# Kernel tuning notes

Hardware: AMD Instinct MI355X
Metric: run time of the kernel (lower is better)

The kernel has to match this reference:

```python
import jax, jax.numpy as jnp
import numpy as np

# Module constants (from init_kwargs / source constants)
BEV_H, BEV_W = 188, 126
IMG_H, IMG_W = 384, 768
X_MIN, X_MAX = 0.0, 75.2
Y_MIN, Y_MAX = -25.2, 25.2


def _bev_points():
    """Homogeneous car-frame BEV cell centers, [P,4] with P = BEV_H*BEV_W, Z=0."""
    dx = (X_MAX - X_MIN) / BEV_H
    dy = (Y_MAX - Y_MIN) / BEV_W
    xc = jnp.linspace(X_MIN + dx / 2.0, X_MAX - dx / 2.0, BEV_H)
    yc = jnp.linspace(Y_MIN + dy / 2.0, Y_MAX - dy / 2.0, BEV_W)
    X, Y = jnp.meshgrid(xc, yc, indexing='ij')
    P = BEV_H * BEV_W
    return jnp.stack([X.ravel(), Y.ravel(), jnp.zeros(P), jnp.ones(P)], axis=-1)


def setup_inputs() -> dict:
    key = jax.random.key(0)
    k1, k2, k3 = jax.random.split(key, 3)
    B, N, C, Hf, Wf = 2, 6, 256, 48, 96
    feats = jax.random.normal(k1, (B, N, C, Hf, Wf), dtype=jnp.float32)
    # Realistic intrinsics: fx=fy=500, principal point at image center, + small noise
    K_base = jnp.array([[500.0, 0.0, IMG_W / 2.0],
                        [0.0, 500.0, IMG_H / 2.0],
                        [0.0, 0.0, 1.0]], dtype=jnp.float32)
    intrinsics = K_base[None, None] + 5.0 * jax.random.normal(k2, (B, N, 3, 3), dtype=jnp.float32)
    intrinsics = intrinsics.at[..., 2, :].set(jnp.array([0.0, 0.0, 1.0]))
    # Extrinsics: car x (forward) -> cam z, car y -> -cam x, car z (up) -> -cam y,
    # camera 1.5m above ground; small per-camera perturbation so cams differ.
    M_base = jnp.array([[0.0, -1.0, 0.0, 0.0],
                        [0.0, 0.0, -1.0, 1.5],
                        [1.0, 0.0, 0.0, 0.0],
                        [0.0, 0.0, 0.0, 1.0]], dtype=jnp.float32)
    car_to_cam = M_base[None, None] + 0.01 * jax.random.normal(k3, (B, N, 4, 4), dtype=jnp.float32)
    car_to_cam = car_to_cam.at[..., 3, :].set(jnp.array([0.0, 0.0, 0.0, 1.0]))
    return {"feats": feats, "intrinsics": intrinsics, "car_to_cam": car_to_cam}


def _forward(feats, intrinsics, car_to_cam):
    B, N, C, Hf, Wf = feats.shape
    P_car = _bev_points().astype(feats.dtype)  # [P,4]
    # Per-camera projection of BEV points into camera frame: P_cam = P_car @ M^T
    P_cam = jnp.einsum('pk,bnjk->bnpj', P_car, car_to_cam)  # [B,N,P,4]
    Zc = P_cam[..., 2]
    valid = Zc > 0.1
    # Pinhole projection: p_img = K @ P_cam3
    p_img = jnp.einsum('bnij,bnpj->bnpi', intrinsics, P_cam[..., :3])  # [B,N,P,3]
    z = jnp.maximum(p_img[..., 2], 1e-4)
    u_feat = (p_img[..., 0] / z) / (IMG_W / float(Wf))
    v_feat = (p_img[..., 1] / z) / (IMG_H / float(Hf))
    valid = valid & (u_feat >= 0.0) & (u_feat <= Wf - 1.0) & (v_feat >= 0.0) & (v_feat <= Hf - 1.0)
    u_norm = jnp.where(valid, u_feat / (Wf - 1) * 2.0 - 1.0, 2.0)
    v_norm = jnp.where(valid, v_feat / (Hf - 1) * 2.0 - 1.0, 2.0)
    # grid_sample, bilinear, padding_mode='zeros', align_corners=True
    ix = (u_norm + 1.0) * 0.5 * (Wf - 1)  # [B,N,P]
    iy = (v_norm + 1.0) * 0.5 * (Hf - 1)
    x0 = jnp.floor(ix)
    y0 = jnp.floor(iy)
    wx1 = ix - x0
    wx0 = 1.0 - wx1
    wy1 = iy - y0
    wy0 = 1.0 - wy1
    feats_flat = feats.reshape(B, N, C, Hf * Wf)

    def gather(xf, yf):
        inb = (xf >= 0) & (xf <= Wf - 1) & (yf >= 0) & (yf <= Hf - 1)
        xi = jnp.clip(xf, 0, Wf - 1).astype(jnp.int32)
        yi = jnp.clip(yf, 0, Hf - 1).astype(jnp.int32)
        lin = yi * Wf + xi  # [B,N,P]
        val = jnp.take_along_axis(feats_flat, lin[:, :, None, :], axis=3)  # [B,N,C,P]
        return val * inb[:, :, None, :].astype(val.dtype)

    out = (gather(x0, y0) * (wx0 * wy0)[:, :, None, :]
           + gather(x0 + 1.0, y0) * (wx1 * wy0)[:, :, None, :]
           + gather(x0, y0 + 1.0) * (wx0 * wy1)[:, :, None, :]
           + gather(x0 + 1.0, y0 + 1.0) * (wx1 * wy1)[:, :, None, :])  # [B,N,C,P]
    bev = out.mean(axis=1).reshape(B, C, BEV_H, BEV_W)
    return bev


def reference(feats, intrinsics, car_to_cam):
    return _forward(feats, intrinsics, car_to_cam)
```

## Files before the change

### kernel.cpp

```cpp
#include <hip/hip_runtime.h>

namespace {

constexpr int kBevH = 188, kBevW = 126, kP = kBevH * kBevW;
constexpr int kB = 2, kN = 6, kC = 256, kHf = 48, kWf = 96;
constexpr int kHW = kHf * kWf;
constexpr int kPixBytes = kC * 2;
constexpr int kPTile = 32;
constexpr int kNTiles = (kP + kPTile - 1) / kPTile;
constexpr size_t kImgBytes  = (size_t)kB * kN * kHW * kC * 2;
constexpr size_t kRecCount  = (size_t)kB * kP * (size_t)kN;
constexpr size_t kOffsBytes = kRecCount * 8;
constexpr size_t kWtsBytes  = kRecCount * 16;
constexpr size_t kWsNeeded  = kImgBytes + kOffsBytes + kWtsBytes;

__device__ __forceinline__ unsigned short f2bf(float f) {
  union { float f; unsigned u; } a; a.f = f;
  unsigned r = a.u + 0x7fffu + ((a.u >> 16) & 1u);
  return (unsigned short)(r >> 16);
}
__device__ __forceinline__ float bfl(unsigned u) {
  union { unsigned u; float f; } a; a.u = u << 16; return a.f;
}
__device__ __forceinline__ float bfh(unsigned u) {
  union { unsigned u; float f; } a; a.u = u & 0xffff0000u; return a.f;
}

__global__ __launch_bounds__(256) void taps_kernel(
    const float* __restrict__ intr, const float* __restrict__ c2c,
    int2* __restrict__ offs, float4* __restrict__ wts) {
  const int gid = blockIdx.x * 256 + threadIdx.x;
  if (gid >= kB * kP) return;
  const int b = gid / kP, p = gid - b * kP;
  const int pi = p / kBevW, pj = p - pi * kBevW;
  const float dx = 75.2f / 188.0f, dy = 50.4f / 126.0f;
  const float xcar = 0.5f * dx + (float)pi * dx;
  const float ycar = -25.2f + 0.5f * dy + (float)pj * dy;
  const float* Kb = intr + (size_t)b * kN * 9;
  const float* Mb = c2c + (size_t)b * kN * 16;
#pragma unroll
  for (int n = 0; n < kN; ++n) {
    const float* M = Mb + n * 16;
    const float* K = Kb + n * 9;
    float Xc = M[0] * xcar + M[1] * ycar + M[3];
    float Yc = M[4] * xcar + M[5] * ycar + M[7];
    float Zc = M[8] * xcar + M[9] * ycar + M[11];
    float u = K[0] * Xc + K[1] * Yc + K[2] * Zc;
    float v = K[3] * Xc + K[4] * Yc + K[5] * Zc;
    float w = K[6] * Xc + K[7] * Yc + K[8] * Zc;
    float z = fmaxf(w, 1e-4f);
    float uf = (u / z) * 0.125f;
    float vf = (v / z) * 0.125f;
    bool valid = (Zc > 0.1f) && (uf >= 0.0f) && (uf <= 95.0f) &&
                 (vf >= 0.0f) && (vf <= 47.0f);
    int2 ov = make_int2(0, 0);
    float4 wv = make_float4(0.f, 0.f, 0.f, 0.f);
    if (valid) {
      float un = (uf / 95.0f) * 2.0f - 1.0f;
      float vn = (vf / 47.0f) * 2.0f - 1.0f;
      float ix = (un + 1.0f) * 0.5f * 95.0f;
      float iy = (vn + 1.0f) * 0.5f * 47.0f;
      float x0f = floorf(ix), y0f = floorf(iy);
      float wx1 = ix - x0f, wx0 = 1.0f - wx1;
      float wy1 = iy - y0f, wy0 = 1.0f - wy1;
      int x0i = (int)x0f;
      int y0i = (int)y0f;
      int xb = min(x0i, 94);
      float h0 = (x0i <= 94) ? wx0 : 0.0f;
      float h1 = (x0i <= 94) ? wx1 : wx0;
      int y1i = min(y0i + 1, 47);
      const int pix = (b * kN + n) * kHW;
      ov.x = (pix + y0i * kWf + xb) * kPixBytes;
      ov.y = (pix + y1i * kWf + xb) * kPixBytes;
      wv = make_float4(h0 * wy0, h1 * wy0, h0 * wy1, h1 * wy1);
    }
    offs[(size_t)gid * kN + n] = ov;
    wts[(size_t)gid * kN + n] = wv;
  }
}

__global__ __launch_bounds__(256) void transpose_cvt_kernel(
    const float* __restrict__ src, unsigned short* __restrict__ dst) {
  __shared__ float tile[64][33];
  const int m = blockIdx.z;
  const int hw0 = blockIdx.x * 32;
  const int c0 = blockIdx.y * 64;
  const float* s = src + (size_t)m * kC * kHW;
  unsigned short* d = dst + (size_t)m * kHW * kC;
  const int hw = threadIdx.x & 31, cl = threadIdx.x >> 5;
#pragma unroll
  for (int k = 0; k < 8; ++k)
    tile[cl + 8 * k][hw] = s[(size_t)(c0 + cl + 8 * k) * kHW + hw0 + hw];
  __syncthreads();
  const int cp = threadIdx.x & 31, hwl = threadIdx.x >> 5;
#pragma unroll
  for (int k = 0; k < 4; ++k) {
    const int h = hwl + 8 * k;
    ushort2 uv;
    uv.x = f2bf(tile[2 * cp][h]);
    uv.y = f2bf(tile[2 * cp + 1][h]);
    *(ushort2*)(d + (size_t)(hw0 + h) * kC + c0 + 2 * cp) = uv;
  }
}

__global__ __launch_bounds__(512) void gather_kernel(
    const unsigned char* __restrict__ tf, const int2* __restrict__ offs,
    const float4* __restrict__ wts, float* __restrict__ out) {
  __shared__ float sm[kPTile][261];
  const int b = blockIdx.y;
  const int orig = blockIdx.x;
  constexpr int q = kNTiles / 8, r = kNTiles % 8;
  const int xcd = orig & 7, idx = orig >> 3;
  const int tile = (xcd < r ? xcd * (q + 1) : r * (q + 1) + (xcd - r) * q) + idx;
  const int p0 = tile * kPTile;
  const int tid = threadIdx.x;
  const int w = tid >> 6, l = tid & 63;
  const int half = l >> 5;
  const int l16 = l << 4;
  const float inv_n = 1.0f / 6.0f;

#pragma unroll 2
  for (int j = 0; j < 4; ++j) {
    const int pl = w * 4 + j;
    const int p = min(p0 + pl, kP - 1);
    int rec = (b * kP + p) * kN;
    rec = __builtin_amdgcn_readfirstlane(rec);

    const int2 o0 = offs[rec + 0], o1 = offs[rec + 1], o2 = offs[rec + 2],
               o3 = offs[rec + 3], o4 = offs[rec + 4], o5 = offs[rec + 5];
    const float4 w0 = wts[rec + 0], w1 = wts[rec + 1], w2 = wts[rec + 2],
                 w3 = wts[rec + 3], w4 = wts[rec + 4], w5 = wts[rec + 5];

#define LD(nm, o) \
    const uint4 nm##a = *(const uint4*)(tf + (size_t)o.x + l16); \
    const uint4 nm##b = *(const uint4*)(tf + (size_t)o.y + l16);
    LD(d0, o0) LD(d1, o1) LD(d2, o2) LD(d3, o3) LD(d4, o4) LD(d5, o5)
#undef LD

    float a0 = 0.f, a1 = 0.f, a2 = 0.f, a3 = 0.f,
          a4 = 0.f, a5 = 0.f, a6 = 0.f, a7 = 0.f;
#define CAM(nm, wv) { \
    const float wA = half ? wv.y : wv.x; \
    const float wB = half ? wv.w : wv.z; \
    a0 += wA * bfl(nm##a.x) + wB * bfl(nm##b.x); \
    a1 += wA * bfh(nm##a.x) + wB * bfh(nm##b.x); \
    a2 += wA * bfl(nm##a.y) + wB * bfl(nm##b.y); \
    a3 += wA * bfh(nm##a.y) + wB * bfh(nm##b.y); \
    a4 += wA * bfl(nm##a.z) + wB * bfl(nm##b.z); \
    a5 += wA * bfh(nm##a.z) + wB * bfh(nm##b.z); \
    a6 += wA * bfl(nm##a.w) + wB * bfl(nm##b.w); \
    a7 += wA * bfh(nm##a.w) + wB * bfh(nm##b.w); }
    CAM(d0, w0) CAM(d1, w1) CAM(d2, w2) CAM(d3, w3) CAM(d4, w4) CAM(d5, w5)
#undef CAM

    a0 += __shfl_xor(a0, 32); a1 += __shfl_xor(a1, 32);
    a2 += __shfl_xor(a2, 32); a3 += __shfl_xor(a3, 32);
    a4 += __shfl_xor(a4, 32); a5 += __shfl_xor(a5, 32);
    a6 += __shfl_xor(a6, 32); a7 += __shfl_xor(a7, 32);

    const int cbase = ((l & 31) << 3) + (half << 2);
    float4 vs = half ? make_float4(a4, a5, a6, a7)
                     : make_float4(a0, a1, a2, a3);
    vs.x *= inv_n; vs.y *= inv_n; vs.z *= inv_n; vs.w *= inv_n;
    *(float4*)&sm[pl][cbase] = vs;
  }
  __syncthreads();

#pragma unroll
  for (int rd = 0; rd < 4; ++rd) {
    const int cr = rd * 64 + (tid >> 3);
    const int p4 = (tid & 7) * 4;
    const int pg = p0 + p4;
    if (pg < kP) {
      float4 v = make_float4(sm[p4][cr], sm[p4 + 1][cr], sm[p4 + 2][cr],
                             sm[p4 + 3][cr]);
      *(float4*)(out + ((size_t)(b * kC + cr)) * kP + pg) = v;
    }
  }
}

constexpr int kCChunk = 32;
__global__ __launch_bounds__(256) void ipm_project_kernel(
    const float* __restrict__ feats, const float* __restrict__ intr,
    const float* __restrict__ c2c, float* __restrict__ out) {
  const int p = blockIdx.x * 256 + threadIdx.x;
  const int b = blockIdx.y;
  const int c0 = blockIdx.z * kCChunk;
  const bool inrange = p < kP;
  const int pi = p / kBevW;
  const int pj = p - pi * kBevW;
  const float dx = 75.2f / 188.0f;
  const float dy = 50.4f / 126.0f;
  const float xcar = 0.5f * dx + (float)pi * dx;
  const float ycar = -25.2f + 0.5f * dy + (float)pj * dy;
  int tap[kN][4];
  float tw[kN][4];
  int vmask = 0;
  const float* Kb = intr + (size_t)b * kN * 9;
  const float* Mb = c2c + (size_t)b * kN * 16;
#pragma unroll
  for (int n = 0; n < kN; ++n) {
    const float* M = Mb + n * 16;
    const float* K = Kb + n * 9;
    float Xc = M[0] * xcar + M[1] * ycar + M[3];
    float Yc = M[4] * xcar + M[5] * ycar + M[7];
    float Zc = M[8] * xcar + M[9] * ycar + M[11];
    float u = K[0] * Xc + K[1] * Yc + K[2] * Zc;
    float v = K[3] * Xc + K[4] * Yc + K[5] * Zc;
    float w = K[6] * Xc + K[7] * Yc + K[8] * Zc;
    float z = fmaxf(w, 1e-4f);
    float uf = (u / z) * 0.125f;
    float vf = (v / z) * 0.125f;
    bool valid = inrange && (Zc > 0.1f) && (uf >= 0.0f) && (uf <= 95.0f) &&
                 (vf >= 0.0f) && (vf <= 47.0f);
    if (valid) {
      float un = (uf / 95.0f) * 2.0f - 1.0f;
      float vn = (vf / 47.0f) * 2.0f - 1.0f;
      float ix = (un + 1.0f) * 0.5f * 95.0f;
      float iy = (vn + 1.0f) * 0.5f * 47.0f;
      float x0f = floorf(ix), y0f = floorf(iy);
      float wx1 = ix - x0f, wx0 = 1.0f - wx1;
      float wy1 = iy - y0f, wy0 = 1.0f - wy1;
#pragma unroll
      for (int t = 0; t < 4; ++t) {
        float xf = x0f + (float)(t & 1);
        float yf = y0f + (float)(t >> 1);
        bool inb =
            (xf >= 0.0f) && (xf <= 95.0f) && (yf >= 0.0f) && (yf <= 47.0f);
        int xi = (int)fminf(fmaxf(xf, 0.0f), 95.0f);
        int yi = (int)fminf(fmaxf(yf, 0.0f), 47.0f);
        float wgt = ((t & 1) ? wx1 : wx0) * ((t >> 1) ? wy1 : wy0);
        tap[n][t] = yi * kWf + xi;
        tw[n][t] = inb ? wgt : 0.0f;
      }
      vmask |= (1 << n);
    }
  }
  const float inv_n = 1.0f / 6.0f;
#pragma unroll 4
  for (int k = 0; k < kCChunk; ++k) {
    const int c = c0 + k;
    float acc = 0.0f;
#pragma unroll
    for (int n = 0; n < kN; ++n) {
      if (vmask & (1 << n)) {
        const float* f = feats + ((size_t)(b * kN + n) * kC + c) * kHW;
        acc += f[tap[n][0]] * tw[n][0] + f[tap[n][1]] * tw[n][1] +
               f[tap[n][2]] * tw[n][2] + f[tap[n][3]] * tw[n][3];
      }
    }
    if (inrange) out[((size_t)b * kC + c) * kP + p] = acc * inv_n;
  }
}

}

extern "C" void kernel_launch(void* const* d_in, const int* in_sizes, int n_in,
                              void* d_out, int out_size, void* d_ws,
                              size_t ws_size, hipStream_t stream) {
  const float* feats = (const float*)d_in[0];
  const float* intr = (const float*)d_in[1];
  const float* c2c = (const float*)d_in[2];
  float* out = (float*)d_out;

  if (ws_size >= kWsNeeded && d_ws != nullptr) {
    unsigned char* wsb = (unsigned char*)d_ws;
    unsigned short* tf = (unsigned short*)wsb;
    int2* offs = (int2*)(wsb + kImgBytes);
    float4* wtsp = (float4*)(wsb + kImgBytes + kOffsBytes);

    taps_kernel<<<(kB * kP + 255) / 256, 256, 0, stream>>>(intr, c2c, offs,
                                                           wtsp);
    transpose_cvt_kernel<<<dim3(kHW / 32, kC / 64, kB * kN), 256, 0, stream>>>(
        feats, tf);
    gather_kernel<<<dim3(kNTiles, kB), 512, 0, stream>>>(
        (const unsigned char*)tf, offs, wtsp, out);
  } else {
    dim3 grid((kP + 255) / 256, kB, kC / kCChunk);
    ipm_project_kernel<<<grid, dim3(256), 0, stream>>>(feats, intr, c2c, out);
  }
}
```

Measured before the change: 54.29 us.

## Fuse tap computation into gather kernel via shared memory, drop taps pass

Removes the separate taps kernel and computes per-point, per-camera offsets and bilinear weights inside the gather kernel. The first 192 threads of each block fill shared-memory arrays, and the rest of the block reads them after a barrier. This drops one kernel launch and the global write and read of the offset and weight records. It also fully unrolls the point loop and switches the output writes to nontemporal stores. The cost is a serial projection phase plus a barrier at the start of every gather block, and higher register pressure from the full unroll.

```diff
diff --git a/kernel.cpp b/kernel.cpp
--- a/kernel.cpp
+++ b/kernel.cpp
@@ -8,11 +8,10 @@
 constexpr int kPixBytes = kC * 2;
 constexpr int kPTile = 32;
 constexpr int kNTiles = (kP + kPTile - 1) / kPTile;
-constexpr size_t kImgBytes  = (size_t)kB * kN * kHW * kC * 2;
-constexpr size_t kRecCount  = (size_t)kB * kP * (size_t)kN;
-constexpr size_t kOffsBytes = kRecCount * 8;
-constexpr size_t kWtsBytes  = kRecCount * 16;
-constexpr size_t kWsNeeded  = kImgBytes + kOffsBytes + kWtsBytes;
+constexpr size_t kImgBytes = (size_t)kB * kN * kHW * kC * 2;
+constexpr size_t kWsNeeded = kImgBytes;
+
+typedef float vfloat4 __attribute__((ext_vector_type(4)));
 
 __device__ __forceinline__ unsigned short f2bf(float f) {
   union { float f; unsigned u; } a; a.f = f;
@@ -26,22 +25,54 @@
   union { unsigned u; float f; } a; a.u = u & 0xffff0000u; return a.f;
 }
 
-__global__ __launch_bounds__(256) void taps_kernel(
-    const float* __restrict__ intr, const float* __restrict__ c2c,
-    int2* __restrict__ offs, float4* __restrict__ wts) {
-  const int gid = blockIdx.x * 256 + threadIdx.x;
-  if (gid >= kB * kP) return;
-  const int b = gid / kP, p = gid - b * kP;
-  const int pi = p / kBevW, pj = p - pi * kBevW;
-  const float dx = 75.2f / 188.0f, dy = 50.4f / 126.0f;
-  const float xcar = 0.5f * dx + (float)pi * dx;
-  const float ycar = -25.2f + 0.5f * dy + (float)pj * dy;
-  const float* Kb = intr + (size_t)b * kN * 9;
-  const float* Mb = c2c + (size_t)b * kN * 16;
-#pragma unroll
-  for (int n = 0; n < kN; ++n) {
-    const float* M = Mb + n * 16;
-    const float* K = Kb + n * 9;
+__global__ __launch_bounds__(256) void transpose_cvt_kernel(
+    const float* __restrict__ src, unsigned short* __restrict__ dst) {
+  __shared__ float tile[64][33];
+  const int m = blockIdx.z;
+  const int hw0 = blockIdx.x * 32;
+  const int c0 = blockIdx.y * 64;
+  const float* s = src + (size_t)m * kC * kHW;
+  unsigned short* d = dst + (size_t)m * kHW * kC;
+  const int hw = threadIdx.x & 31, cl = threadIdx.x >> 5;
+#pragma unroll
+  for (int k = 0; k < 8; ++k)
+    tile[cl + 8 * k][hw] = s[(size_t)(c0 + cl + 8 * k) * kHW + hw0 + hw];
+  __syncthreads();
+  const int cp = threadIdx.x & 31, hwl = threadIdx.x >> 5;
+#pragma unroll
+  for (int k = 0; k < 4; ++k) {
+    const int h = hwl + 8 * k;
+    ushort2 uv;
+    uv.x = f2bf(tile[2 * cp][h]);
+    uv.y = f2bf(tile[2 * cp + 1][h]);
+    *(ushort2*)(d + (size_t)(hw0 + h) * kC + c0 + 2 * cp) = uv;
+  }
+}
+
+__global__ __launch_bounds__(512) void gather_kernel(
+    const unsigned char* __restrict__ tf, const float* __restrict__ intr,
+    const float* __restrict__ c2c, float* __restrict__ out) {
+  __shared__ float sm[kPTile][261];
+  __shared__ int2 s_off[kPTile][kN];
+  __shared__ float4 s_wt[kPTile][kN];
+
+  const int b = blockIdx.y;
+  const int orig = blockIdx.x;
+  constexpr int q = kNTiles / 8, r = kNTiles % 8;
+  const int xcd = orig & 7, idx = orig >> 3;
+  const int tile = (xcd < r ? xcd * (q + 1) : r * (q + 1) + (xcd - r) * q) + idx;
+  const int p0 = tile * kPTile;
+  const int tid = threadIdx.x;
+
+  if (tid < kPTile * kN) {
+    const int pl = tid / kN, n = tid - pl * kN;
+    const int p = min(p0 + pl, kP - 1);
+    const int pi = p / kBevW, pj = p - pi * kBevW;
+    const float dxc = 75.2f / 188.0f, dyc = 50.4f / 126.0f;
+    const float xcar = 0.5f * dxc + (float)pi * dxc;
+    const float ycar = -25.2f + 0.5f * dyc + (float)pj * dyc;
+    const float* M = c2c + ((size_t)b * kN + n) * 16;
+    const float* K = intr + ((size_t)b * kN + n) * 9;
     float Xc = M[0] * xcar + M[1] * ycar + M[3];
     float Yc = M[4] * xcar + M[5] * ycar + M[7];
     float Zc = M[8] * xcar + M[9] * ycar + M[11];
@@ -74,62 +105,24 @@
       ov.y = (pix + y1i * kWf + xb) * kPixBytes;
       wv = make_float4(h0 * wy0, h1 * wy0, h0 * wy1, h1 * wy1);
     }
-    offs[(size_t)gid * kN + n] = ov;
-    wts[(size_t)gid * kN + n] = wv;
-  }
-}
-
-__global__ __launch_bounds__(256) void transpose_cvt_kernel(
-    const float* __restrict__ src, unsigned short* __restrict__ dst) {
-  __shared__ float tile[64][33];
-  const int m = blockIdx.z;
-  const int hw0 = blockIdx.x * 32;
-  const int c0 = blockIdx.y * 64;
-  const float* s = src + (size_t)m * kC * kHW;
-  unsigned short* d = dst + (size_t)m * kHW * kC;
-  const int hw = threadIdx.x & 31, cl = threadIdx.x >> 5;
-#pragma unroll
-  for (int k = 0; k < 8; ++k)
-    tile[cl + 8 * k][hw] = s[(size_t)(c0 + cl + 8 * k) * kHW + hw0 + hw];
+    s_off[pl][n] = ov;
+    s_wt[pl][n] = wv;
+  }
   __syncthreads();
-  const int cp = threadIdx.x & 31, hwl = threadIdx.x >> 5;
-#pragma unroll
-  for (int k = 0; k < 4; ++k) {
-    const int h = hwl + 8 * k;
-    ushort2 uv;
-    uv.x = f2bf(tile[2 * cp][h]);
-    uv.y = f2bf(tile[2 * cp + 1][h]);
-    *(ushort2*)(d + (size_t)(hw0 + h) * kC + c0 + 2 * cp) = uv;
-  }
-}
-
-__global__ __launch_bounds__(512) void gather_kernel(
-    const unsigned char* __restrict__ tf, const int2* __restrict__ offs,
-    const float4* __restrict__ wts, float* __restrict__ out) {
-  __shared__ float sm[kPTile][261];
-  const int b = blockIdx.y;
-  const int orig = blockIdx.x;
-  constexpr int q = kNTiles / 8, r = kNTiles % 8;
-  const int xcd = orig & 7, idx = orig >> 3;
-  const int tile = (xcd < r ? xcd * (q + 1) : r * (q + 1) + (xcd - r) * q) + idx;
-  const int p0 = tile * kPTile;
-  const int tid = threadIdx.x;
+
   const int w = tid >> 6, l = tid & 63;
   const int half = l >> 5;
   const int l16 = l << 4;
   const float inv_n = 1.0f / 6.0f;
 
-#pragma unroll 2
+#pragma unroll
   for (int j = 0; j < 4; ++j) {
     const int pl = w * 4 + j;
-    const int p = min(p0 + pl, kP - 1);
-    int rec = (b * kP + p) * kN;
-    rec = __builtin_amdgcn_readfirstlane(rec);
-
-    const int2 o0 = offs[rec + 0], o1 = offs[rec + 1], o2 = offs[rec + 2],
-               o3 = offs[rec + 3], o4 = offs[rec + 4], o5 = offs[rec + 5];
-    const float4 w0 = wts[rec + 0], w1 = wts[rec + 1], w2 = wts[rec + 2],
-                 w3 = wts[rec + 3], w4 = wts[rec + 4], w5 = wts[rec + 5];
+
+    const int2 o0 = s_off[pl][0], o1 = s_off[pl][1], o2 = s_off[pl][2],
+               o3 = s_off[pl][3], o4 = s_off[pl][4], o5 = s_off[pl][5];
+    const float4 q0 = s_wt[pl][0], q1 = s_wt[pl][1], q2 = s_wt[pl][2],
+                 q3 = s_wt[pl][3], q4 = s_wt[pl][4], q5 = s_wt[pl][5];
 
 #define LD(nm, o) \
     const uint4 nm##a = *(const uint4*)(tf + (size_t)o.x + l16); \
@@ -139,18 +132,19 @@
 
     float a0 = 0.f, a1 = 0.f, a2 = 0.f, a3 = 0.f,
           a4 = 0.f, a5 = 0.f, a6 = 0.f, a7 = 0.f;
-#define CAM(nm, wv) { \
-    const float wA = half ? wv.y : wv.x; \
-    const float wB = half ? wv.w : wv.z; \
-    a0 += wA * bfl(nm##a.x) + wB * bfl(nm##b.x); \
-    a1 += wA * bfh(nm##a.x) + wB * bfh(nm##b.x); \
-    a2 += wA * bfl(nm##a.y) + wB * bfl(nm##b.y); \
-    a3 += wA * bfh(nm##a.y) + wB * bfh(nm##b.y); \
-    a4 += wA * bfl(nm##a.z) + wB * bfl(nm##b.z); \
-    a5 += wA * bfh(nm##a.z) + wB * bfh(nm##b.z); \
-    a6 += wA * bfl(nm##a.w) + wB * bfl(nm##b.w); \
-    a7 += wA * bfh(nm##a.w) + wB * bfh(nm##b.w); }
-    CAM(d0, w0) CAM(d1, w1) CAM(d2, w2) CAM(d3, w3) CAM(d4, w4) CAM(d5, w5)
+#define CAM(da, db, wv) { \
+    const float selA = half ? wv.y : wv.x; \
+    const float selB = half ? wv.w : wv.z; \
+    a0 += selA * bfl(da.x) + selB * bfl(db.x); \
+    a1 += selA * bfh(da.x) + selB * bfh(db.x); \
+    a2 += selA * bfl(da.y) + selB * bfl(db.y); \
+    a3 += selA * bfh(da.y) + selB * bfh(db.y); \
+    a4 += selA * bfl(da.z) + selB * bfl(db.z); \
+    a5 += selA * bfh(da.z) + selB * bfh(db.z); \
+    a6 += selA * bfl(da.w) + selB * bfl(db.w); \
+    a7 += selA * bfh(da.w) + selB * bfh(db.w); }
+    CAM(d0a, d0b, q0) CAM(d1a, d1b, q1) CAM(d2a, d2b, q2)
+    CAM(d3a, d3b, q3) CAM(d4a, d4b, q4) CAM(d5a, d5b, q5)
 #undef CAM
 
     a0 += __shfl_xor(a0, 32); a1 += __shfl_xor(a1, 32);
@@ -172,9 +166,10 @@
     const int p4 = (tid & 7) * 4;
     const int pg = p0 + p4;
     if (pg < kP) {
-      float4 v = make_float4(sm[p4][cr], sm[p4 + 1][cr], sm[p4 + 2][cr],
-                             sm[p4 + 3][cr]);
-      *(float4*)(out + ((size_t)(b * kC + cr)) * kP + pg) = v;
+      vfloat4 v = {sm[p4][cr], sm[p4 + 1][cr], sm[p4 + 2][cr],
+                   sm[p4 + 3][cr]};
+      __builtin_nontemporal_store(
+          v, (vfloat4*)(out + ((size_t)(b * kC + cr)) * kP + pg));
     }
   }
 }
@@ -264,17 +259,11 @@
   float* out = (float*)d_out;
 
   if (ws_size >= kWsNeeded && d_ws != nullptr) {
-    unsigned char* wsb = (unsigned char*)d_ws;
-    unsigned short* tf = (unsigned short*)wsb;
-    int2* offs = (int2*)(wsb + kImgBytes);
-    float4* wtsp = (float4*)(wsb + kImgBytes + kOffsBytes);
-
-    taps_kernel<<<(kB * kP + 255) / 256, 256, 0, stream>>>(intr, c2c, offs,
-                                                           wtsp);
+    unsigned short* tf = (unsigned short*)d_ws;
     transpose_cvt_kernel<<<dim3(kHW / 32, kC / 64, kB * kN), 256, 0, stream>>>(
         feats, tf);
     gather_kernel<<<dim3(kNTiles, kB), 512, 0, stream>>>(
-        (const unsigned char*)tf, offs, wtsp, out);
+        (const unsigned char*)tf, intr, c2c, out);
   } else {
     dim3 grid((kP + 255) / 256, kB, kC / kCChunk);
     ipm_project_kernel<<<grid, dim3(256), 0, stream>>>(feats, intr, c2c, out);
```

After: 49.20 us. 1.1x faster.
